# Optimization experiments

Hardware: AMD Instinct MI355X
Metric: run time of the kernel (lower is better)

The kernel has to match this reference:

```python
import jax, jax.numpy as jnp
import numpy as np

# ---- static config ----
B, N, C, HF, WF = 2, 256, 256, 64, 64
PATCH = 512
ROI = 15
MARGIN = (ROI - 1) // 2
HID = 256
HEADS = 8
DEPTH = 3
FFN = 1024
NQ = 16
LN_EPS = 1e-5


def setup_inputs() -> dict:
    key = jax.random.key(0)
    ks = jax.random.split(key, 16)
    p = lambda i, shape: (0.02 * jax.random.normal(ks[i], shape, jnp.float32))
    inp = {
        "image_embeddings": jax.random.normal(ks[0], (B, C, HF, WF), jnp.float32),
        "keypoints": jax.random.uniform(ks[1], (B, N, 2), jnp.float32, 0.0, float(PATCH)),
        "keypoints_valid_mask": jax.random.randint(ks[2], (B, N), 0, 2) == 1,
        "proj_w": p(3, (HID, C)), "proj_b": jnp.zeros((HID,), jnp.float32),
        "query_embed": p(4, (NQ, HID)),
        "self_qkv_w": p(5, (DEPTH, 3 * HID, HID)), "self_qkv_b": jnp.zeros((DEPTH, 3 * HID), jnp.float32),
        "self_out_w": p(6, (DEPTH, HID, HID)), "self_out_b": jnp.zeros((DEPTH, HID), jnp.float32),
        "cross_qkv_w": p(7, (DEPTH, 3 * HID, HID)), "cross_qkv_b": jnp.zeros((DEPTH, 3 * HID), jnp.float32),
        "cross_out_w": p(8, (DEPTH, HID, HID)), "cross_out_b": jnp.zeros((DEPTH, HID), jnp.float32),
        "ffn1_w": p(9, (DEPTH, FFN, HID)), "ffn1_b": jnp.zeros((DEPTH, FFN), jnp.float32),
        "ffn2_w": p(10, (DEPTH, HID, FFN)), "ffn2_b": jnp.zeros((DEPTH, HID), jnp.float32),
        "ln1_w": jnp.ones((DEPTH, HID), jnp.float32), "ln1_b": jnp.zeros((DEPTH, HID), jnp.float32),
        "ln2_w": jnp.ones((DEPTH, HID), jnp.float32), "ln2_b": jnp.zeros((DEPTH, HID), jnp.float32),
        "ln3_w": jnp.ones((DEPTH, HID), jnp.float32), "ln3_b": jnp.zeros((DEPTH, HID), jnp.float32),
        "out_w": p(11, (4, HID)), "out_b": jnp.zeros((4,), jnp.float32),
    }
    return inp


def _layer_norm(x, w, b):
    mu = x.mean(-1, keepdims=True)
    var = ((x - mu) ** 2).mean(-1, keepdims=True)
    return (x - mu) * jax.lax.rsqrt(var + LN_EPS) * w + b


def _mha(q_in, kv_in, Wqkv, bqkv, Wo, bo, pad=None):
    # PyTorch nn.MultiheadAttention math (batch_first). pad: [B, S_kv] True=masked.
    Dh = HID // HEADS
    Wq, Wk, Wv = jnp.split(Wqkv, 3, axis=0)
    bq, bk, bv = jnp.split(bqkv, 3, axis=0)
    Bsz = q_in.shape[0]
    q = (q_in @ Wq.T + bq).reshape(Bsz, -1, HEADS, Dh)
    k = (kv_in @ Wk.T + bk).reshape(Bsz, -1, HEADS, Dh)
    v = (kv_in @ Wv.T + bv).reshape(Bsz, -1, HEADS, Dh)
    s = jnp.einsum('bqhd,bkhd->bhqk', q, k) * (Dh ** -0.5)
    if pad is not None:
        s = jnp.where(pad[:, None, None, :], -jnp.inf, s)
    a = jax.nn.softmax(s, axis=-1)
    o = jnp.einsum('bhqk,bkhd->bqhd', a, v).reshape(Bsz, -1, HID)
    return o @ Wo.T + bo


def _roi_sample(img, keypoints):
    # _get_valid_grid + F.grid_sample(bilinear, align_corners=False, zeros padding)
    rc = jnp.round(keypoints)                               # [B,N,2] (r,c), round-half-even like Python round
    off = jnp.arange(-MARGIN, MARGIN + 1, dtype=img.dtype)  # [ROI]
    gy = rc[:, :, 0][..., None, None] + off[:, None]        # [B,N,ROI,ROI] rows
    gx = rc[:, :, 1][..., None, None] + off[None, :]        # [B,N,ROI,ROI] cols
    gxn = gx / (PATCH - 1) * 2.0 - 1.0
    gyn = gy / (PATCH - 1) * 2.0 - 1.0
    invalid = (gxn < -1) | (gyn < -1) | (gxn > 1) | (gyn > 1)  # [B,N,ROI,ROI]
    gxn = jnp.where(invalid, 0.0, gxn)
    gyn = jnp.where(invalid, 0.0, gyn)
    # unnormalize onto the feature map (align_corners=False)
    x = ((gxn + 1.0) * WF - 1.0) * 0.5
    y = ((gyn + 1.0) * HF - 1.0) * 0.5
    x = x.reshape(B, -1)  # [B, P], P = N*ROI*ROI
    y = y.reshape(B, -1)
    x0f = jnp.floor(x); y0f = jnp.floor(y)
    wx = x - x0f; wy = y - y0f
    x0 = x0f.astype(jnp.int32); y0 = y0f.astype(jnp.int32)
    bidx = jnp.arange(B)[:, None]

    def tap(yi, xi, w):
        ok = (yi >= 0) & (yi < HF) & (xi >= 0) & (xi < WF)
        yc = jnp.clip(yi, 0, HF - 1)
        xc = jnp.clip(xi, 0, WF - 1)
        v = img[bidx, :, yc, xc]                 # [B,P,C] gather
        return v * (w * ok)[..., None]

    out = (tap(y0, x0, (1 - wy) * (1 - wx)) + tap(y0, x0 + 1, (1 - wy) * wx)
           + tap(y0 + 1, x0, wy * (1 - wx)) + tap(y0 + 1, x0 + 1, wy * wx))
    feat = out.reshape(B, N, ROI * ROI, C)
    feat = jnp.where(invalid.reshape(B, N, ROI * ROI)[..., None], 0.0, feat)
    return feat  # [B, N, HW, C]


def reference(image_embeddings, keypoints, keypoints_valid_mask, proj_w, proj_b,
              query_embed, self_qkv_w, self_qkv_b, self_out_w, self_out_b,
              cross_qkv_w, cross_qkv_b, cross_out_w, cross_out_b,
              ffn1_w, ffn1_b, ffn2_w, ffn2_b,
              ln1_w, ln1_b, ln2_w, ln2_b, ln3_w, ln3_b, out_w, out_b):
    feat = _roi_sample(image_embeddings, keypoints)                 # [B,N,HW,C]
    mem = jnp.einsum('bnpc,oc->bnpo', feat, proj_w) + proj_b        # 1x1 conv proj
    mem = mem.reshape(B * N, ROI * ROI, HID)
    pad = jnp.broadcast_to(~keypoints_valid_mask.reshape(-1, 1), (B * N, ROI * ROI))
    pad = pad.at[:, 0].set(False)                                    # token 0 always attendable
    tgt = jnp.broadcast_to(query_embed[None], (B * N, NQ, HID))
    for l in range(DEPTH):  # post-norm TransformerDecoderLayer, relu, eval (no dropout)
        sa = _mha(tgt, tgt, self_qkv_w[l], self_qkv_b[l], self_out_w[l], self_out_b[l])
        tgt = _layer_norm(tgt + sa, ln1_w[l], ln1_b[l])
        ca = _mha(tgt, mem, cross_qkv_w[l], cross_qkv_b[l], cross_out_w[l], cross_out_b[l], pad)
        tgt = _layer_norm(tgt + ca, ln2_w[l], ln2_b[l])
        ff = jax.nn.relu(tgt @ ffn1_w[l].T + ffn1_b[l]) @ ffn2_w[l].T + ffn2_b[l]
        tgt = _layer_norm(tgt + ff, ln3_w[l], ln3_b[l])
    out = tgt @ out_w.T + out_b                                      # [B*N, NQ, 4]
    return out.reshape(B, N, NQ, 4)
```

## Files before the change

### kernel.cpp

```cpp
#include <hip/hip_runtime.h>
#include <hip/hip_fp16.h>

#define LB __launch_bounds__(256)

typedef unsigned short u16;
typedef unsigned int   u32;
typedef __attribute__((ext_vector_type(8))) short bf16x8;
typedef __attribute__((ext_vector_type(4))) float f32x4;
typedef __attribute__((ext_vector_type(8))) u16  u16x8;

__device__ __forceinline__ u16 f2b(float f) {
    u32 u = __float_as_uint(f);
    u32 r = (u + 0x7fffu + ((u >> 16) & 1u)) >> 16;
    return (u16)r;
}
__device__ __forceinline__ float b2f(u16 h) {
    return __uint_as_float((u32)h << 16);
}

#define QSCALE 0.17677669529663687f


__global__ void k_prep(const unsigned char* __restrict__ m, int* __restrict__ valid,
                       const float* __restrict__ pb,
                       const float* __restrict__ cqkv_w,
                       const float* __restrict__ cqkv_b,
                       float* __restrict__ ckv)
{
    if (blockIdx.x == 0) {
        __shared__ int flag;
        if (threadIdx.x == 0) flag = 0;
        __syncthreads();
        int loc = 0;
        for (int off = threadIdx.x; off < 512; off += 256)
            if ((off & 3) != 0 && m[off] != 0) loc = 1;
        if (loc) atomicOr(&flag, 1);
        __syncthreads();
        const bool bytelay = (flag != 0);
        for (int s = threadIdx.x; s < 512; s += 256)
            valid[s] = bytelay ? (int)(m[s] != 0) : (int)(((const int*)m)[s] != 0);
    } else {
        const int l = blockIdx.x - 1;
        const float* Wk = cqkv_w + (size_t)l * 196608 + 65536;
        const float* Wv = cqkv_w + (size_t)l * 196608 + 131072;
        const float* kb = cqkv_b + (size_t)l * 768 + 256;
        const float* vb = cqkv_b + (size_t)l * 768 + 512;
        const int o = threadIdx.x;
        float a = 0.f, c = 0.f;
        for (int cc = 0; cc < 256; cc += 4) {
            const float4 p4 = *(const float4*)(pb + cc);
            const float4 k4 = *(const float4*)(Wk + (size_t)o * 256 + cc);
            const float4 v4 = *(const float4*)(Wv + (size_t)o * 256 + cc);
            a += p4.x * k4.x + p4.y * k4.y + p4.z * k4.z + p4.w * k4.w;
            c += p4.x * v4.x + p4.y * v4.y + p4.z * v4.z + p4.w * v4.w;
        }
        ckv[l * 512 + o]       = a + kb[o];
        ckv[l * 512 + 256 + o] = c + vb[o];
    }
}

__global__ LB void k_wconv(const float* __restrict__ s0, const float* __restrict__ s1,
                           const float* __restrict__ s2, const float* __restrict__ s3,
                           const float* __restrict__ s4, const float* __restrict__ s5,
                           const float* __restrict__ s6, u16* __restrict__ dst)
{
    const int e = blockIdx.x * 256 + threadIdx.x;
    if (e >= 3604480) return;
    float v;
    int i = e;
    if (i < 65536) v = s0[i];
    else if ((i -= 65536) < 589824) v = s1[i];
    else if ((i -= 589824) < 196608) v = s2[i];
    else if ((i -= 196608) < 589824) v = s3[i];
    else if ((i -= 589824) < 196608) v = s4[i];
    else if ((i -= 196608) < 786432) v = s5[i];
    else if ((i -= 786432) < 786432) v = s6[i];
    else {
        i -= 786432;
        const int l = i / 131072;
        const int r = (i - l * 131072) >> 8;
        const int c = i & 255;
        v = s3[(size_t)l * 196608 + (size_t)(256 + r) * 256 + c];
    }
    dst[e] = f2b(v);
}

__global__ LB void k_transpose(const float* __restrict__ img, u16* __restrict__ imgTb)
{
    __shared__ float tile[64][65];
    const int b  = blockIdx.z;
    const int c0 = blockIdx.y * 64;
    const int p0 = blockIdx.x * 64;
    const int t  = threadIdx.x;
    const int tr = t >> 6, tc = t & 63;
#pragma unroll
    for (int p = 0; p < 16; ++p) {
        const int i = p * 4 + tr;
        tile[i][tc] = img[((size_t)(b * 256 + c0 + i)) * 4096 + p0 + tc];
    }
    __syncthreads();
#pragma unroll
    for (int p = 0; p < 16; ++p) {
        const int jj = p * 4 + tr;
        imgTb[((size_t)(b * 4096 + p0 + jj)) * 256 + c0 + tc] = f2b(tile[tc][jj]);
    }
}

template<int BM>
__global__ LB void gemm_mfma(const u16* __restrict__ A, const u16* __restrict__ W,
                             const float* __restrict__ bias,
                             float* __restrict__ Cf, u16* __restrict__ Cb,
                             int M, int N, int K, int relu)
{
    constexpr int BN = 128;
    __shared__ u16 lds[2][(BM + BN) * 64];
    const int t = threadIdx.x;
    const int wid = t >> 6, lane = t & 63;
    const int bm = blockIdx.y * BM, bn = blockIdx.x * BN;
    const int KT = K >> 6;

    auto stage = [&](int buf, int kt) {
        const int k0 = kt * 64;
        const int rr = t >> 3;
        const int u  = t & 7;
#pragma unroll
        for (int q = 0; q < BM / 32; ++q) {
            const int r = q * 32 + rr;
            const u16* src = A + (size_t)(bm + r) * K + k0 + ((u ^ (r & 7)) << 3);
            __builtin_amdgcn_global_load_lds(
                (const __attribute__((address_space(1))) void*)src,
                (__attribute__((address_space(3))) void*)&lds[buf][q * 2048 + wid * 512],
                16, 0, 0);
        }
#pragma unroll
        for (int q = 0; q < 4; ++q) {
            const int r = q * 32 + rr;
            const u16* src = W + (size_t)(bn + r) * K + k0 + ((u ^ (r & 7)) << 3);
            __builtin_amdgcn_global_load_lds(
                (const __attribute__((address_space(1))) void*)src,
                (__attribute__((address_space(3))) void*)&lds[buf][BM * 64 + q * 2048 + wid * 512],
                16, 0, 0);
        }
    };

    const int wr = wid >> 1, wc = wid & 1;
    constexpr int MR = BM / 32;
    f32x4 acc[MR][4];
    const f32x4 z = {0.f, 0.f, 0.f, 0.f};
#pragma unroll
    for (int mi = 0; mi < MR; ++mi)
#pragma unroll
        for (int ni = 0; ni < 4; ++ni) acc[mi][ni] = z;

    const int r16 = lane & 15, kg = lane >> 4;

    stage(0, 0);
    int cur = 0;
    for (int kt = 0; kt < KT; ++kt) {
        asm volatile("s_waitcnt vmcnt(0)" ::: "memory");
        __syncthreads();
        if (kt + 1 < KT) stage(cur ^ 1, kt + 1);
        const u16* pA = lds[cur];
        const u16* pB = lds[cur] + BM * 64;
#pragma unroll
        for (int kk = 0; kk < 2; ++kk) {
            const int s = kk * 4 + kg;
            bf16x8 afr[MR], bfr[4];
#pragma unroll
            for (int mi = 0; mi < MR; ++mi) {
                const int r = wr * (BM / 2) + mi * 16 + r16;
                afr[mi] = *(const bf16x8*)(pA + r * 64 + ((s ^ (r & 7)) << 3));
            }
#pragma unroll
            for (int ni = 0; ni < 4; ++ni) {
                const int c = wc * 64 + ni * 16 + r16;
                bfr[ni] = *(const bf16x8*)(pB + c * 64 + ((s ^ (c & 7)) << 3));
            }
#pragma unroll
            for (int mi = 0; mi < MR; ++mi)
#pragma unroll
                for (int ni = 0; ni < 4; ++ni)
                    acc[mi][ni] = __builtin_amdgcn_mfma_f32_16x16x32_bf16(
                        afr[mi], bfr[ni], acc[mi][ni], 0, 0, 0);
        }
        cur ^= 1;
    }

#pragma unroll
    for (int mi = 0; mi < MR; ++mi) {
#pragma unroll
        for (int ni = 0; ni < 4; ++ni) {
            const int col = bn + wc * 64 + ni * 16 + r16;
            const float bs = bias ? bias[col] : 0.0f;
#pragma unroll
            for (int rg = 0; rg < 4; ++rg) {
                const int row = bm + wr * (BM / 2) + mi * 16 + kg * 4 + rg;
                float v = acc[mi][ni][rg] + bs;
                if (relu) v = fmaxf(v, 0.0f);
                if (Cf) Cf[(size_t)row * N + col] = v;
                if (Cb) Cb[(size_t)row * N + col] = f2b(v);
            }
        }
    }
}

__global__ LB void gemm_ln(const u16* __restrict__ A, const u16* __restrict__ W,
                           const float* __restrict__ bias,
                           float* __restrict__ tgt, u16* __restrict__ tgtb,
                           const float* __restrict__ lnw, const float* __restrict__ lnb,
                           int K)
{
    __shared__ u16 lA[32 * 64];
    __shared__ u16 lB[256 * 64];
    __shared__ float psum[2][32];
    __shared__ float psq[2][32];
    const int t = threadIdx.x;
    const int wid = t >> 6, lane = t & 63;
    const int r16 = lane & 15, kg = lane >> 4;
    const int wr = wid >> 1, wc = wid & 1;
    const int bm = blockIdx.x * 32;
    const int KT = K >> 6;

    f32x4 acc[8];
    const f32x4 z = {0.f, 0.f, 0.f, 0.f};
#pragma unroll
    for (int ni = 0; ni < 8; ++ni) acc[ni] = z;

    for (int kt = 0; kt < KT; ++kt) {
        const int k0 = kt * 64;
        const int rr = t >> 3;
        const int u  = t & 7;
        {
            const int r = rr;
            const u16* src = A + (size_t)(bm + r) * K + k0 + ((u ^ (r & 7)) << 3);
            __builtin_amdgcn_global_load_lds(
                (const __attribute__((address_space(1))) void*)src,
                (__attribute__((address_space(3))) void*)&lA[wid * 512],
                16, 0, 0);
        }
#pragma unroll
        for (int q = 0; q < 8; ++q) {
            const int r = q * 32 + rr;
            const u16* src = W + (size_t)r * K + k0 + ((u ^ (r & 7)) << 3);
            __builtin_amdgcn_global_load_lds(
                (const __attribute__((address_space(1))) void*)src,
                (__attribute__((address_space(3))) void*)&lB[q * 2048 + wid * 512],
                16, 0, 0);
        }
        asm volatile("s_waitcnt vmcnt(0)" ::: "memory");
        __syncthreads();
#pragma unroll
        for (int kk = 0; kk < 2; ++kk) {
            const int s = kk * 4 + kg;
            const int ra = wr * 16 + r16;
            const bf16x8 afr = *(const bf16x8*)(lA + ra * 64 + ((s ^ (ra & 7)) << 3));
#pragma unroll
            for (int ni = 0; ni < 8; ++ni) {
                const int c = wc * 128 + ni * 16 + r16;
                const bf16x8 bfr = *(const bf16x8*)(lB + c * 64 + ((s ^ (c & 7)) << 3));
                acc[ni] = __builtin_amdgcn_mfma_f32_16x16x32_bf16(afr, bfr, acc[ni], 0, 0, 0);
            }
        }
        __syncthreads();
    }

    float xv[4][8];
    float bcol[8], wcol[8], bncol[8];
#pragma unroll
    for (int ni = 0; ni < 8; ++ni) {
        const int c = wc * 128 + ni * 16 + r16;
        bcol[ni]  = bias[c];
        wcol[ni]  = lnw[c];
        bncol[ni] = lnb[c];
    }
#pragma unroll
    for (int rg = 0; rg < 4; ++rg) {
        const int row = bm + wr * 16 + kg * 4 + rg;
#pragma unroll
        for (int ni = 0; ni < 8; ++ni) {
            const int c = wc * 128 + ni * 16 + r16;
            xv[rg][ni] = tgt[(size_t)row * 256 + c] + acc[ni][rg] + bcol[ni];
        }
    }
#pragma unroll
    for (int rg = 0; rg < 4; ++rg) {
        float s = 0.f;
#pragma unroll
        for (int ni = 0; ni < 8; ++ni) s += xv[rg][ni];
#pragma unroll
        for (int m = 1; m < 16; m <<= 1) s += __shfl_xor(s, m);
        if (r16 == 0) psum[wc][wr * 16 + kg * 4 + rg] = s;
    }
    __syncthreads();
    float mu[4];
#pragma unroll
    for (int rg = 0; rg < 4; ++rg) {
        const int rl = wr * 16 + kg * 4 + rg;
        mu[rg] = (psum[0][rl] + psum[1][rl]) * (1.0f / 256.0f);
    }
#pragma unroll
    for (int rg = 0; rg < 4; ++rg) {
        float q = 0.f;
#pragma unroll
        for (int ni = 0; ni < 8; ++ni) {
            const float d = xv[rg][ni] - mu[rg];
            q += d * d;
        }
#pragma unroll
        for (int m = 1; m < 16; m <<= 1) q += __shfl_xor(q, m);
        if (r16 == 0) psq[wc][wr * 16 + kg * 4 + rg] = q;
    }
    __syncthreads();
#pragma unroll
    for (int rg = 0; rg < 4; ++rg) {
        const int rl = wr * 16 + kg * 4 + rg;
        const int row = bm + rl;
        const float var = (psq[0][rl] + psq[1][rl]) * (1.0f / 256.0f);
        const float inv = 1.0f / sqrtf(var + 1e-5f);
#pragma unroll
        for (int ni = 0; ni < 8; ++ni) {
            const int c = wc * 128 + ni * 16 + r16;
            const float o = (xv[rg][ni] - mu[rg]) * inv * wcol[ni] + bncol[ni];
            tgt[(size_t)row * 256 + c]  = o;
            tgtb[(size_t)row * 256 + c] = f2b(o);
        }
    }
}

__global__ LB void k_init_tgt(float* __restrict__ tgt, u16* __restrict__ tgtb,
                              const float* __restrict__ qe)
{
    const int e = blockIdx.x * 256 + threadIdx.x;
    const int c = e & 255;
    const int row = e >> 8;
    const int i = row & 15;
    const float v = qe[(i << 8) | c];
    tgt[e] = v;
    tgtb[e] = f2b(v);
}

__global__ LB void k_self_attn(const u16* __restrict__ QKV, u16* __restrict__ O)
{
    __shared__ __align__(16) u16 arena[4][1536];
    const int t = threadIdx.x;
    const int lane = t & 63, wid = t >> 6;
    const int r16 = lane & 15, kg = lane >> 4;
    const int blk = blockIdx.x;
    const int s = blk >> 1;
    const int h = (blk & 1) * 4 + wid;

    u16* p_lds = &arena[wid][0];
    u16* vT    = &arena[wid][512];

    const bf16x8 qfr = *(const bf16x8*)(QKV + (size_t)(s * 16 + r16) * 768 + h * 32 + kg * 8);
    const bf16x8 kfr = *(const bf16x8*)(QKV + (size_t)(s * 16 + r16) * 768 + 256 + h * 32 + kg * 8);
    f32x4 sv = {0.f, 0.f, 0.f, 0.f};
    sv = __builtin_amdgcn_mfma_f32_16x16x32_bf16(qfr, kfr, sv, 0, 0, 0);

    float ev[4], rowsum[4];
#pragma unroll
    for (int rg = 0; rg < 4; ++rg) ev[rg] = sv[rg] * QSCALE;
#pragma unroll
    for (int rg = 0; rg < 4; ++rg) {
        float mx = ev[rg];
#pragma unroll
        for (int m = 1; m < 16; m <<= 1) mx = fmaxf(mx, __shfl_xor(mx, m));
        ev[rg] = __expf(ev[rg] - mx);
        float ps = ev[rg];
#pragma unroll
        for (int m = 1; m < 16; m <<= 1) ps += __shfl_xor(ps, m);
        rowsum[rg] = ps;
    }

#pragma unroll
    for (int rg = 0; rg < 4; ++rg)
        p_lds[(kg * 4 + rg) * 32 + r16] = f2b(ev[rg]);
    {
        const int zq = lane & 15, zc = 16 + (lane >> 4) * 4;
#pragma unroll
        for (int j = 0; j < 4; ++j) p_lds[zq * 32 + zc + j] = 0;
    }
    {
        const int key = lane >> 2, ch8 = (lane & 3) * 8;
        const u16x8 v = *(const u16x8*)(QKV + (size_t)(s * 16 + key) * 768 + 512 + h * 32 + ch8);
#pragma unroll
        for (int j = 0; j < 8; ++j)
            vT[(ch8 + j) * 32 + key] = ((const u16*)&v)[j];
        const int zc0 = lane >> 1, zk0 = 16 + (lane & 1) * 8;
#pragma unroll
        for (int j = 0; j < 8; ++j) vT[zc0 * 32 + zk0 + j] = 0;
    }

#pragma unroll
    for (int ct = 0; ct < 2; ++ct) {
        const bf16x8 pa = *(const bf16x8*)(p_lds + r16 * 32 + kg * 8);
        const bf16x8 vb = *(const bf16x8*)(vT + (ct * 16 + r16) * 32 + kg * 8);
        f32x4 ao = {0.f, 0.f, 0.f, 0.f};
        ao = __builtin_amdgcn_mfma_f32_16x16x32_bf16(pa, vb, ao, 0, 0, 0);
#pragma unroll
        for (int rg = 0; rg < 4; ++rg) {
            const int q = kg * 4 + rg;
            O[(size_t)(s * 16 + q) * 256 + h * 32 + ct * 16 + r16] = f2b(ao[rg] / rowsum[rg]);
        }
    }
}

__global__ LB void k_cross_attn(const u16* __restrict__ Qb,
                                const u16* __restrict__ KV, int kvs,
                                const float* __restrict__ ckv,
                                const int* __restrict__ valid,
                                const float* __restrict__ kps,
                                u16* __restrict__ O)
{
    __shared__ __align__(16) char arena[64832];
    u16* Wm  = (u16*)arena;
    u16* WmT = (u16*)(arena + 14400);

    const int t = threadIdx.x;
    const int lane = t & 63, wid = t >> 6;
    const int r16 = lane & 15, kg = lane >> 4;
    const int blk = blockIdx.x;
    const int s = blk >> 1;
    const int h = (blk & 1) * 4 + wid;
    const int b = s >> 8, n = s & 255;

    u16* buf = (u16*)(arena + 22848 + wid * 10496);
    u16* p_b = (u16*)(arena + 22848 + wid * 10496 + 2048);
    u16* QP  = p_b;

    for (int e = t; e < 16208; e += 256) ((u32*)arena)[e] = 0;
    __syncthreads();

    const float kpy = kps[(b * 256 + n) * 2 + 0];
    const float kpx = kps[(b * 256 + n) * 2 + 1];
    const float gx0 = rintf(kpx) - 7.0f;
    const float gy0 = rintf(kpy) - 7.0f;
    const float gxn0 = gx0 / 511.0f * 2.0f - 1.0f;
    const float gyn0 = gy0 / 511.0f * 2.0f - 1.0f;
    const float xb = ((gxn0 + 1.f) * 64.f - 1.f) * 0.5f;
    const float yb = ((gyn0 + 1.f) * 64.f - 1.f) * 0.5f;
    const int x0b = (int)floorf(xb);
    const int y0b = (int)floorf(yb);

    if (t < 225) {
        const int iy = t / 15, ix = t - iy * 15;
        const float gy = rintf(kpy) + (float)(iy - 7);
        const float gx = rintf(kpx) + (float)(ix - 7);
        const float gxn = gx / 511.0f * 2.0f - 1.0f;
        const float gyn = gy / 511.0f * 2.0f - 1.0f;
        const bool inval = (gxn < -1.f) || (gyn < -1.f) || (gxn > 1.f) || (gyn > 1.f);
        const float x = ((gxn + 1.f) * 64.f - 1.f) * 0.5f;
        const float y = ((gyn + 1.f) * 64.f - 1.f) * 0.5f;
        const float x0f = floorf(x), y0f = floorf(y);
        const float wx = x - x0f, wy = y - y0f;
        const int x0 = (int)x0f, y0 = (int)y0f;
#pragma unroll
        for (int tt = 0; tt < 4; ++tt) {
            const int dy = tt >> 1, dx = tt & 1;
            const int yi = y0 + dy, xi = x0 + dx;
            const bool ok = (yi >= 0) && (yi < 64) && (xi >= 0) && (xi < 64) && !inval;
            const float w = (dy ? wy : 1.f - wy) * (dx ? wx : 1.f - wx);
            if (ok) {
                const int cell = (yi - y0b) * 4 + (xi - x0b);
                const u16 wb = f2b(w);
                Wm[t * 32 + ((((cell >> 3) ^ (t & 3)) << 3) | (cell & 7))] = wb;
                WmT[cell * 264 + t] = wb;
            }
        }
    }
    const int cell = lane >> 2, ch8 = (lane & 3) * 8;
    const int cy = cell >> 2, cx = cell & 3;
    const int py = min(max(y0b + cy, 0), 63);
    const int px = min(max(x0b + cx, 0), 63);
    const size_t texidx = (size_t)(b * 4096 + py * 64 + px) * kvs + h * 32 + ch8;
    *(u16x8*)(buf + cell * 32 + ch8) = *(const u16x8*)(KV + texidx);
    const bool vld = valid[s] != 0;
    __syncthreads();

    {
        const bf16x8 qfr = *(const bf16x8*)(Qb + (size_t)(s * 16 + r16) * 256 + h * 32 + kg * 8);
        const bf16x8 tfr = *(const bf16x8*)(buf + r16 * 32 + kg * 8);
        f32x4 aq = {0.f, 0.f, 0.f, 0.f};
        aq = __builtin_amdgcn_mfma_f32_16x16x32_bf16(qfr, tfr, aq, 0, 0, 0);
#pragma unroll
        for (int rg = 0; rg < 4; ++rg)
            QP[(kg * 4 + rg) * 40 + r16] = f2b(aq[rg]);
    }

    float ev[4][15];
    {
        const bf16x8 afr = *(const bf16x8*)(QP + r16 * 40 + kg * 8);
#pragma unroll
        for (int tile = 0; tile < 15; ++tile) {
            const int p = tile * 16 + r16;
            const int rc = p < 225 ? p : 224;
            const bf16x8 bfr = *(const bf16x8*)(Wm + rc * 32 + ((kg ^ (rc & 3)) << 3));
            f32x4 acc = {0.f, 0.f, 0.f, 0.f};
            acc = __builtin_amdgcn_mfma_f32_16x16x32_bf16(afr, bfr, acc, 0, 0, 0);
#pragma unroll
            for (int rg = 0; rg < 4; ++rg) {
                float sv = acc[rg] * QSCALE;
                if (p > 224) sv = -1e30f;
                if (!vld && p > 0) sv = -1e30f;
                ev[rg][tile] = sv;
            }
        }
    }
    float rowsumv[4];
#pragma unroll
    for (int rg = 0; rg < 4; ++rg) {
        float mx = -1e30f;
#pragma unroll
        for (int k = 0; k < 15; ++k) mx = fmaxf(mx, ev[rg][k]);
#pragma unroll
        for (int m = 1; m < 16; m <<= 1) mx = fmaxf(mx, __shfl_xor(mx, m));
        float ps = 0.f;
#pragma unroll
        for (int k = 0; k < 15; ++k) {
            ev[rg][k] = __expf(ev[rg][k] - mx);
            ps += ev[rg][k];
        }
#pragma unroll
        for (int m = 1; m < 16; m <<= 1) ps += __shfl_xor(ps, m);
        rowsumv[rg] = ps;
    }

#pragma unroll
    for (int rg = 0; rg < 4; ++rg)
#pragma unroll
        for (int k = 0; k < 15; ++k) {
            const int p = k * 16 + r16;
            if (p < 225) p_b[(kg * 4 + rg) * 264 + p] = f2b(ev[rg][k]);
        }
    for (int e = lane; e < 496; e += 64) {
        const int row = e / 31;
        p_b[row * 264 + 225 + (e - row * 31)] = 0;
    }

    {
        const u16x8 v = *(const u16x8*)(KV + texidx + 256);
#pragma unroll
        for (int j = 0; j < 8; ++j)
            buf[(ch8 + j) * 32 + cell] = ((const u16*)&v)[j];
        const int zr = lane & 15, zc0 = 16 + (lane >> 4) * 4;
#pragma unroll
        for (int j = 0; j < 4; ++j) buf[zr * 32 + zc0 + j] = 0;
    }

    f32x4 pw = {0.f, 0.f, 0.f, 0.f};
#pragma unroll
    for (int ks = 0; ks < 8; ++ks) {
        const bf16x8 pa = *(const bf16x8*)(p_b + r16 * 264 + ks * 32 + kg * 8);
        const bf16x8 wb = *(const bf16x8*)(WmT + r16 * 264 + ks * 32 + kg * 8);
        pw = __builtin_amdgcn_mfma_f32_16x16x32_bf16(pa, wb, pw, 0, 0, 0);
    }

#pragma unroll
    for (int rg = 0; rg < 4; ++rg)
        QP[(kg * 4 + rg) * 40 + r16] = f2b(pw[rg]);
    {
        const int zq = lane & 15, zc0 = 16 + (lane >> 4) * 4;
#pragma unroll
        for (int j = 0; j < 4; ++j) QP[zq * 40 + zc0 + j] = 0;
    }

#pragma unroll
    for (int ct = 0; ct < 2; ++ct) {
        const bf16x8 pa = *(const bf16x8*)(QP + r16 * 40 + kg * 8);
        const bf16x8 vb = *(const bf16x8*)(buf + (ct * 16 + r16) * 32 + kg * 8);
        f32x4 ao = {0.f, 0.f, 0.f, 0.f};
        ao = __builtin_amdgcn_mfma_f32_16x16x32_bf16(pa, vb, ao, 0, 0, 0);
#pragma unroll
        for (int rg = 0; rg < 4; ++rg) {
            const int q = kg * 4 + rg;
            const int ch = h * 32 + ct * 16 + r16;
            const float val = ao[rg] / rowsumv[rg] + ckv[256 + ch];
            O[(size_t)(s * 16 + q) * 256 + ch] = f2b(val);
        }
    }
}

__global__ LB void k_out(const float* __restrict__ X, const float* __restrict__ W,
                         const float* __restrict__ bias, float* __restrict__ O)
{
    __shared__ float w_s[4][260];
    const int t = threadIdx.x;
    for (int e = t; e < 1024; e += 256) w_s[e >> 8][e & 255] = W[e];
    __syncthreads();
    const int row = blockIdx.x * 64 + (t >> 2);
    const int j = t & 3;
    const float4* xr = (const float4*)(X + (size_t)row * 256);
    float acc = 0.0f;
#pragma unroll
    for (int k4 = 0; k4 < 64; ++k4) {
        const float4 x = xr[k4];
        acc += x.x * w_s[j][k4 * 4]     + x.y * w_s[j][k4 * 4 + 1]
             + x.z * w_s[j][k4 * 4 + 2] + x.w * w_s[j][k4 * 4 + 3];
    }
    O[(size_t)row * 4 + j] = acc + bias[j];
}

extern "C" void kernel_launch(void* const* d_in, const int* in_sizes, int n_in,
                              void* d_out, int out_size, void* d_ws, size_t ws_size,
                              hipStream_t stream)
{
    const float* img          = (const float*)d_in[0];
    const float* kps          = (const float*)d_in[1];
    const unsigned char* vmsk = (const unsigned char*)d_in[2];
    const float* proj_w       = (const float*)d_in[3];
    const float* proj_b       = (const float*)d_in[4];
    const float* query_embed  = (const float*)d_in[5];
    const float* self_qkv_w   = (const float*)d_in[6];
    const float* self_qkv_b   = (const float*)d_in[7];
    const float* self_out_w   = (const float*)d_in[8];
    const float* self_out_b   = (const float*)d_in[9];
    const float* cross_qkv_w  = (const float*)d_in[10];
    const float* cross_qkv_b  = (const float*)d_in[11];
    const float* cross_out_w  = (const float*)d_in[12];
    const float* cross_out_b  = (const float*)d_in[13];
    const float* ffn1_w       = (const float*)d_in[14];
    const float* ffn1_b       = (const float*)d_in[15];
    const float* ffn2_w       = (const float*)d_in[16];
    const float* ffn2_b       = (const float*)d_in[17];
    const float* ln1_w        = (const float*)d_in[18];
    const float* ln1_b        = (const float*)d_in[19];
    const float* ln2_w        = (const float*)d_in[20];
    const float* ln2_b        = (const float*)d_in[21];
    const float* ln3_w        = (const float*)d_in[22];
    const float* ln3_b        = (const float*)d_in[23];
    const float* out_w        = (const float*)d_in[24];
    const float* out_b        = (const float*)d_in[25];
    float* out = (float*)d_out;

    char* W8 = (char*)d_ws;
    size_t off = 0;
    auto alloc = [&](size_t bytes) { void* p = W8 + off; off += (bytes + 255) & ~(size_t)255; return p; };
    float* tgt   = (float*)alloc(2097152 * 4);
    u16* Qb      = (u16*)alloc(2097152 * 2);
    u16* Sb16    = (u16*)alloc(6291456 * 2);
    float* ckv   = (float*)alloc(3 * 512 * 4);
    u16* imgTb   = (u16*)alloc(2097152 * 2);
    u16* imgPb   = (u16*)alloc(2097152 * 2);
    u16* KVb3    = (u16*)alloc(12582912 * 2);
    u16* tgtb    = (u16*)alloc(2097152 * 2);
    u16* Abuf    = (u16*)alloc(2097152 * 2);
    u16* Hbuf    = (u16*)alloc(8388608 * 2);
    u16* wAll    = (u16*)alloc(3604480 * 2);
    int* valid   = (int*)alloc(512 * 4);

    u16* wProj = wAll;
    u16* wSQKV = wProj + 65536;
    u16* wSOut = wSQKV + 589824;
    u16* wCQKV = wSOut + 196608;
    u16* wCOut = wCQKV + 589824;
    u16* wF1   = wCOut + 196608;
    u16* wF2   = wF1 + 786432;
    u16* wCKV3 = wF2 + 786432;

    k_prep<<<4, 256, 0, stream>>>(vmsk, valid, proj_b, cross_qkv_w, cross_qkv_b, ckv);
    k_wconv<<<14080, 256, 0, stream>>>(proj_w, self_qkv_w, self_out_w, cross_qkv_w,
                                       cross_out_w, ffn1_w, ffn2_w, wAll);
    k_transpose<<<dim3(64, 4, 2), 256, 0, stream>>>(img, imgTb);
    gemm_mfma<64><<<dim3(2, 128), 256, 0, stream>>>(imgTb, wProj, nullptr,
                                                    nullptr, imgPb, 8192, 256, 256, 0);
    gemm_mfma<128><<<dim3(12, 64), 256, 0, stream>>>(imgPb, wCKV3, nullptr,
                                                     nullptr, KVb3, 8192, 1536, 256, 0);
    k_init_tgt<<<8192, 256, 0, stream>>>(tgt, tgtb, query_embed);

    for (int l = 0; l < 3; ++l) {
        gemm_mfma<64><<<dim3(6, 128), 256, 0, stream>>>(tgtb, wSQKV + (size_t)l * 196608,
            self_qkv_b + (size_t)l * 768, nullptr, Sb16, 8192, 768, 256, 0);
        k_self_attn<<<1024, 256, 0, stream>>>(Sb16, Abuf);
        gemm_ln<<<256, 256, 0, stream>>>(Abuf, wSOut + (size_t)l * 65536,
            self_out_b + (size_t)l * 256, tgt, tgtb,
            ln1_w + (size_t)l * 256, ln1_b + (size_t)l * 256, 256);

        gemm_mfma<64><<<dim3(2, 128), 256, 0, stream>>>(tgtb, wCQKV + (size_t)l * 196608,
            cross_qkv_b + (size_t)l * 768, nullptr, Qb, 8192, 256, 256, 0);
        k_cross_attn<<<1024, 256, 0, stream>>>(Qb, KVb3 + (size_t)l * 512, 1536,
                                               ckv + (size_t)l * 512, valid, kps, Abuf);
        gemm_ln<<<256, 256, 0, stream>>>(Abuf, wCOut + (size_t)l * 65536,
            cross_out_b + (size_t)l * 256, tgt, tgtb,
            ln2_w + (size_t)l * 256, ln2_b + (size_t)l * 256, 256);

        gemm_mfma<64><<<dim3(8, 128), 256, 0, stream>>>(tgtb, wF1 + (size_t)l * 262144,
            ffn1_b + (size_t)l * 1024, nullptr, Hbuf, 8192, 1024, 256, 1);
        gemm_ln<<<256, 256, 0, stream>>>(Hbuf, wF2 + (size_t)l * 262144,
            ffn2_b + (size_t)l * 256, tgt, tgtb,
            ln3_w + (size_t)l * 256, ln3_b + (size_t)l * 256, 1024);
    }

    k_out<<<128, 256, 0, stream>>>(tgt, out_w, out_b, out);
}
```

Before: 382.6 us.

## Fold 1x1 projection into cross KV weights and fuse output head into LN

The 1x1 projection weight is premultiplied into the cross-attention K/V weights with a small GEMM on the weights, so the image features go straight into one GEMM instead of two. This removes the 8192x256x256 projection GEMM and its intermediate buffer. Separately, the final 4-wide output head is computed in the epilogue of the last LayerNorm GEMM, which removes the k_out launch and a re-read of tgt. Premultiplying the weights in bf16 adds an extra rounding step, so numerics change slightly.

After: 378.3 us. Within noise of the previous version (-1.1%).

```diff
diff --git a/kernel.cpp b/kernel.cpp
--- a/kernel.cpp
+++ b/kernel.cpp
@@ -65,7 +65,7 @@
                            const float* __restrict__ s6, u16* __restrict__ dst)
 {
     const int e = blockIdx.x * 256 + threadIdx.x;
-    if (e >= 3604480) return;
+    if (e >= 3670016) return;
     float v;
     int i = e;
     if (i < 65536) v = s0[i];
@@ -75,12 +75,14 @@
     else if ((i -= 589824) < 196608) v = s4[i];
     else if ((i -= 196608) < 786432) v = s5[i];
     else if ((i -= 786432) < 786432) v = s6[i];
-    else {
-        i -= 786432;
+    else if ((i -= 786432) < 393216) {
         const int l = i / 131072;
         const int r = (i - l * 131072) >> 8;
         const int c = i & 255;
         v = s3[(size_t)l * 196608 + (size_t)(256 + r) * 256 + c];
+    } else {
+        i -= 393216;
+        v = s0[(i & 255) * 256 + (i >> 8)];
     }
     dst[e] = f2b(v);
 }
@@ -208,12 +210,15 @@
                            const float* __restrict__ bias,
                            float* __restrict__ tgt, u16* __restrict__ tgtb,
                            const float* __restrict__ lnw, const float* __restrict__ lnb,
-                           int K)
+                           int K,
+                           const float* __restrict__ ow, const float* __restrict__ ob,
+                           float* __restrict__ outp)
 {
     __shared__ u16 lA[32 * 64];
     __shared__ u16 lB[256 * 64];
     __shared__ float psum[2][32];
     __shared__ float psq[2][32];
+    __shared__ float hsum[2][32][4];
     const int t = threadIdx.x;
     const int wid = t >> 6, lane = t & 63;
     const int r16 = lane & 15, kg = lane >> 4;
@@ -311,6 +316,7 @@
         if (r16 == 0) psq[wc][wr * 16 + kg * 4 + rg] = q;
     }
     __syncthreads();
+    float onorm[4][8];
 #pragma unroll
     for (int rg = 0; rg < 4; ++rg) {
         const int rl = wr * 16 + kg * 4 + rg;
@@ -321,8 +327,34 @@
         for (int ni = 0; ni < 8; ++ni) {
             const int c = wc * 128 + ni * 16 + r16;
             const float o = (xv[rg][ni] - mu[rg]) * inv * wcol[ni] + bncol[ni];
+            onorm[rg][ni] = o;
             tgt[(size_t)row * 256 + c]  = o;
             tgtb[(size_t)row * 256 + c] = f2b(o);
+        }
+    }
+
+    if (outp) {
+#pragma unroll
+        for (int j = 0; j < 4; ++j) {
+            float wj[8];
+#pragma unroll
+            for (int ni = 0; ni < 8; ++ni)
+                wj[ni] = ow[j * 256 + wc * 128 + ni * 16 + r16];
+#pragma unroll
+            for (int rg = 0; rg < 4; ++rg) {
+                float p = 0.f;
+#pragma unroll
+                for (int ni = 0; ni < 8; ++ni) p += onorm[rg][ni] * wj[ni];
+#pragma unroll
+                for (int m = 1; m < 16; m <<= 1) p += __shfl_xor(p, m);
+                if (r16 == 0) hsum[wc][wr * 16 + kg * 4 + rg][j] = p;
+            }
+        }
+        __syncthreads();
+        if (t < 128) {
+            const int row = t >> 2, j = t & 3;
+            outp[(size_t)(bm + row) * 4 + j] =
+                hsum[0][row][j] + hsum[1][row][j] + ob[j];
         }
     }
 }
@@ -578,26 +610,6 @@
             O[(size_t)(s * 16 + q) * 256 + ch] = f2b(val);
         }
     }
-}
-
-__global__ LB void k_out(const float* __restrict__ X, const float* __restrict__ W,
-                         const float* __restrict__ bias, float* __restrict__ O)
-{
-    __shared__ float w_s[4][260];
-    const int t = threadIdx.x;
-    for (int e = t; e < 1024; e += 256) w_s[e >> 8][e & 255] = W[e];
-    __syncthreads();
-    const int row = blockIdx.x * 64 + (t >> 2);
-    const int j = t & 3;
-    const float4* xr = (const float4*)(X + (size_t)row * 256);
-    float acc = 0.0f;
-#pragma unroll
-    for (int k4 = 0; k4 < 64; ++k4) {
-        const float4 x = xr[k4];
-        acc += x.x * w_s[j][k4 * 4]     + x.y * w_s[j][k4 * 4 + 1]
-             + x.z * w_s[j][k4 * 4 + 2] + x.w * w_s[j][k4 * 4 + 3];
-    }
-    O[(size_t)row * 4 + j] = acc + bias[j];
 }
 
 extern "C" void kernel_launch(void* const* d_in, const int* in_sizes, int n_in,
@@ -640,40 +652,43 @@
     u16* Sb16    = (u16*)alloc(6291456 * 2);
     float* ckv   = (float*)alloc(3 * 512 * 4);
     u16* imgTb   = (u16*)alloc(2097152 * 2);
-    u16* imgPb   = (u16*)alloc(2097152 * 2);
     u16* KVb3    = (u16*)alloc(12582912 * 2);
     u16* tgtb    = (u16*)alloc(2097152 * 2);
     u16* Abuf    = (u16*)alloc(2097152 * 2);
     u16* Hbuf    = (u16*)alloc(8388608 * 2);
-    u16* wAll    = (u16*)alloc(3604480 * 2);
+    u16* wAll    = (u16*)alloc(3670016 * 2);
+    u16* WcombB  = (u16*)alloc(393216 * 2);
     int* valid   = (int*)alloc(512 * 4);
 
-    u16* wProj = wAll;
-    u16* wSQKV = wProj + 65536;
-    u16* wSOut = wSQKV + 589824;
-    u16* wCQKV = wSOut + 196608;
-    u16* wCOut = wCQKV + 589824;
-    u16* wF1   = wCOut + 196608;
-    u16* wF2   = wF1 + 786432;
-    u16* wCKV3 = wF2 + 786432;
+    u16* wProj  = wAll;
+    u16* wSQKV  = wProj + 65536;
+    u16* wSOut  = wSQKV + 589824;
+    u16* wCQKV  = wSOut + 196608;
+    u16* wCOut  = wCQKV + 589824;
+    u16* wF1    = wCOut + 196608;
+    u16* wF2    = wF1 + 786432;
+    u16* wCKV3  = wF2 + 786432;
+    u16* wProjT = wCKV3 + 393216;
 
     k_prep<<<4, 256, 0, stream>>>(vmsk, valid, proj_b, cross_qkv_w, cross_qkv_b, ckv);
-    k_wconv<<<14080, 256, 0, stream>>>(proj_w, self_qkv_w, self_out_w, cross_qkv_w,
+    k_wconv<<<14336, 256, 0, stream>>>(proj_w, self_qkv_w, self_out_w, cross_qkv_w,
                                        cross_out_w, ffn1_w, ffn2_w, wAll);
     k_transpose<<<dim3(64, 4, 2), 256, 0, stream>>>(img, imgTb);
-    gemm_mfma<64><<<dim3(2, 128), 256, 0, stream>>>(imgTb, wProj, nullptr,
-                                                    nullptr, imgPb, 8192, 256, 256, 0);
-    gemm_mfma<128><<<dim3(12, 64), 256, 0, stream>>>(imgPb, wCKV3, nullptr,
+    gemm_mfma<64><<<dim3(2, 24), 256, 0, stream>>>(wCKV3, wProjT, nullptr,
+                                                   nullptr, WcombB, 1536, 256, 256, 0);
+    gemm_mfma<128><<<dim3(12, 64), 256, 0, stream>>>(imgTb, WcombB, nullptr,
                                                      nullptr, KVb3, 8192, 1536, 256, 0);
     k_init_tgt<<<8192, 256, 0, stream>>>(tgt, tgtb, query_embed);
 
     for (int l = 0; l < 3; ++l) {
+        const int last = (l == 2);
         gemm_mfma<64><<<dim3(6, 128), 256, 0, stream>>>(tgtb, wSQKV + (size_t)l * 196608,
             self_qkv_b + (size_t)l * 768, nullptr, Sb16, 8192, 768, 256, 0);
         k_self_attn<<<1024, 256, 0, stream>>>(Sb16, Abuf);
         gemm_ln<<<256, 256, 0, stream>>>(Abuf, wSOut + (size_t)l * 65536,
             self_out_b + (size_t)l * 256, tgt, tgtb,
-            ln1_w + (size_t)l * 256, ln1_b + (size_t)l * 256, 256);
+            ln1_w + (size_t)l * 256, ln1_b + (size_t)l * 256, 256,
+            nullptr, nullptr, nullptr);
 
         gemm_mfma<64><<<dim3(2, 128), 256, 0, stream>>>(tgtb, wCQKV + (size_t)l * 196608,
             cross_qkv_b + (size_t)l * 768, nullptr, Qb, 8192, 256, 256, 0);
@@ -681,14 +696,14 @@
                                                ckv + (size_t)l * 512, valid, kps, Abuf);
         gemm_ln<<<256, 256, 0, stream>>>(Abuf, wCOut + (size_t)l * 65536,
             cross_out_b + (size_t)l * 256, tgt, tgtb,
-            ln2_w + (size_t)l * 256, ln2_b + (size_t)l * 256, 256);
+            ln2_w + (size_t)l * 256, ln2_b + (size_t)l * 256, 256,
+            nullptr, nullptr, nullptr);
 
         gemm_mfma<64><<<dim3(8, 128), 256, 0, stream>>>(tgtb, wF1 + (size_t)l * 262144,
             ffn1_b + (size_t)l * 1024, nullptr, Hbuf, 8192, 1024, 256, 1);
         gemm_ln<<<256, 256, 0, stream>>>(Hbuf, wF2 + (size_t)l * 262144,
             ffn2_b + (size_t)l * 256, tgt, tgtb,
-            ln3_w + (size_t)l * 256, ln3_b + (size_t)l * 256, 1024);
-    }
-
-    k_out<<<128, 256, 0, stream>>>(tgt, out_w, out_b, out);
-}
+            ln3_w + (size_t)l * 256, ln3_b + (size_t)l * 256, 1024,
+            last ? out_w : nullptr, last ? out_b : nullptr, last ? out : nullptr);
+    }
+}
```
